# Kernel tuning notes

Hardware: AMD Instinct MI355X
Metric: run time of the kernel (lower is better)

## Reference

```python
import jax, jax.numpy as jnp
import numpy as np

N_E = 4096
E_DIM = 256
DECAY = 0.99
EPS = 1e-5


def setup_inputs() -> dict:
    key = jax.random.key(0)
    k1, k2 = jax.random.split(key)
    z = jax.random.normal(k1, (8, 256, 16, 16, 16), dtype=jnp.float32)
    embedding = jax.random.normal(k2, (N_E, E_DIM), dtype=jnp.float32)
    return {
        "z": z,
        "embedding": embedding,
        "cluster_size": jnp.zeros((N_E,), dtype=jnp.float32),
        "embedding_avg": embedding,  # buffer initialized as embedding.clone()
    }


def reference(z, embedding, cluster_size, embedding_avg):
    n_e, e_dim = embedding.shape
    # b c h w d -> b h w d c, then flatten tokens
    zt = jnp.einsum('bchwd->bhwdc', z)
    zf = zt.reshape(-1, e_dim)                      # [N, e_dim]
    # squared euclidean distances: ||z||^2 + ||e||^2 - 2 z.e
    d = (jnp.sum(zf * zf, axis=1, keepdims=True)
         + jnp.sum(embedding * embedding, axis=1)
         - 2.0 * jnp.einsum('bd,nd->bn', zf, embedding))  # [N, n_e]
    idx = jnp.argmin(d, axis=1)                     # [N]
    # EMA statistics (equivalent to one-hot.T reductions, done via scatter)
    n_total = jnp.zeros((n_e,), zf.dtype).at[idx].add(1.0)          # encodings.sum(0)
    dw = jax.ops.segment_sum(zf, idx, num_segments=n_e)             # encodings.T @ zf
    new_cluster = cluster_size * DECAY + (1.0 - DECAY) * n_total
    new_avg = embedding_avg * DECAY + (1.0 - DECAY) * dw
    n = new_cluster.sum()
    cs = (new_cluster + EPS) / (n + n_e * EPS) * n
    new_embed = new_avg / cs[:, None]
    # quantize (gather == one-hot @ embedding) with straight-through estimator
    zq = jnp.take(embedding, idx, axis=0).reshape(zt.shape)
    zq = zt + jax.lax.stop_gradient(zq - zt)
    zq = jnp.einsum('bhwdc->bchwd', zq)
    usage = (n_total > 0).sum().astype(jnp.float32) / n_e
    return zq, idx, new_cluster, new_avg, new_embed, usage
```

## Files before the change

### kernel.cpp

```cpp
#include <hip/hip_runtime.h>

#define N_E   4096
#define E_DIM 256
#define NTOK  32768
#define ZX    4096
#define DECAY 0.99f
#define EPSV  1e-5f
#define TAU   0.3f
#define NJB   32
#define NHALF 64
#define NSPL  4
#define IBIG  0x7fffffff

typedef _Float16 half8 __attribute__((ext_vector_type(8)));
typedef __attribute__((ext_vector_type(4))) float f32x4;

__device__ __forceinline__ unsigned short f2h(float x) {
    _Float16 h = (_Float16)x;
    unsigned short u;
    __builtin_memcpy(&u, &h, 2);
    return u;
}
__device__ __forceinline__ float h2f(unsigned short u) {
    _Float16 h;
    __builtin_memcpy(&h, &u, 2);
    return (float)h;
}
__device__ __forceinline__ unsigned umin2(unsigned a, unsigned b) { return a < b ? a : b; }
__device__ __forceinline__ unsigned umax2(unsigned a, unsigned b) { return a > b ? a : b; }
__device__ __forceinline__ void gload16(const void* g, void* l) {
    __builtin_amdgcn_global_load_lds(
        (const __attribute__((address_space(1))) char*)g,
        (__attribute__((address_space(3))) char*)l, 16, 0, 0);
}

__global__ void k_prep(const float* __restrict__ z, unsigned short* __restrict__ zh,
                       const float* __restrict__ emb, unsigned short* __restrict__ Bp,
                       float* __restrict__ enorm32, double* __restrict__ enorm64,
                       int* __restrict__ cnt, int* __restrict__ flagCnt,
                       int* __restrict__ flagCnt2) {
    __shared__ float lt[64][65];
    const int tid = threadIdx.x;
    if (blockIdx.x < 2048) {
        const int bid = blockIdx.x;
        const int xt = bid & 63, ct = (bid >> 6) & 3, b = bid >> 8;
        #pragma unroll
        for (int r = 0; r < 4; ++r) {
            int cy = r * 16 + (tid >> 4);
            int xx4 = tid & 15;
            float4 v = ((const float4*)z)[(size_t)(b * 256 + ct * 64 + cy) * 1024 + xt * 16 + xx4];
            lt[cy][xx4 * 4 + 0] = v.x; lt[cy][xx4 * 4 + 1] = v.y;
            lt[cy][xx4 * 4 + 2] = v.z; lt[cy][xx4 * 4 + 3] = v.w;
        }
        __syncthreads();
        #pragma unroll
        for (int it = 0; it < 2; ++it) {
            int tl = it * 32 + (tid >> 3);
            int c8 = tid & 7;
            unsigned short h[8];
            #pragma unroll
            for (int u = 0; u < 8; ++u) h[u] = f2h(lt[c8 * 8 + u][tl]);
            size_t t = (size_t)(b * 4096 + xt * 64 + tl);
            size_t o = t * 256 + ct * 64 + c8 * 8;
            *(ushort4*)&zh[o]     = make_ushort4(h[0], h[1], h[2], h[3]);
            *(ushort4*)&zh[o + 4] = make_ushort4(h[4], h[5], h[6], h[7]);
        }
    } else {
        const int eb = blockIdx.x - 2048;
        if (tid < 4) cnt[eb * 4 + tid] = 0;
        if (eb == 0 && tid == 0) { *flagCnt = 0; *flagCnt2 = 0; }
        int j = eb * 4 + (tid >> 6);
        int lane = tid & 63;
        float4 v = ((const float4*)emb)[(size_t)j * 64 + lane];
        float f[4] = {v.x, v.y, v.z, v.w};
        unsigned short h[4];
        #pragma unroll
        for (int u = 0; u < 4; ++u) h[u] = f2h(f[u]);
        *(ushort4*)&Bp[(size_t)j * E_DIM + lane * 4] = make_ushort4(h[0], h[1], h[2], h[3]);
        double s = 0.0;
        #pragma unroll
        for (int u = 0; u < 4; ++u) s += (double)f[u] * (double)f[u];
        #pragma unroll
        for (int off = 32; off; off >>= 1) s += __shfl_down(s, off, 64);
        if (lane == 0) { enorm32[j] = (float)s; enorm64[j] = s; }
    }
}

__global__ __launch_bounds__(256) void k_dist(
        const unsigned short* __restrict__ zh,
        const unsigned short* __restrict__ Bp, const float* __restrict__ enorm32,
        unsigned* __restrict__ pk1, unsigned* __restrict__ pk2, unsigned* __restrict__ pk3) {
    __shared__ __align__(16) char smem[32768];
    const int tid = threadIdx.x;
    const int lane = tid & 63;
    const int w = tid >> 6;
    const int wr = w >> 1, wc = w & 1;
    const int t0 = blockIdx.x * 128;
    const int jb = blockIdx.y;
    const int j0 = jb * 128;
    const int sw16 = (((lane & 7) ^ (lane >> 3)) << 4);
    const int rowsub = lane >> 3;

    f32x4 acc[4][4];
    #pragma unroll
    for (int m = 0; m < 4; ++m)
        #pragma unroll
        for (int nn = 0; nn < 4; ++nn)
            acc[m][nn] = (f32x4){0.f, 0.f, 0.f, 0.f};

    auto stage = [&](int s) {
        const int kb = s * 128 + sw16;
        #pragma unroll
        for (int c = 0; c < 4; ++c) {
            int seg = w * 4 + c;
            int arow = t0 + seg * 8 + rowsub;
            int brow = j0 + seg * 8 + rowsub;
            gload16((const char*)zh + (size_t)arow * 512 + kb, &smem[seg * 1024]);
            gload16((const char*)Bp + (size_t)brow * 512 + kb, &smem[16384 + seg * 1024]);
        }
    };

    stage(0);
    for (int s = 0; s < 4; ++s) {
        __syncthreads();
        const int xr = ((lane & 7) << 4);
        #pragma unroll
        for (int kk = 0; kk < 2; ++kk) {
            const int colb = (kk * 64 + ((lane >> 4) << 4)) ^ xr;
            half8 a[4], b[4];
            #pragma unroll
            for (int m = 0; m < 4; ++m)
                a[m] = *(const half8*)&smem[((wr * 64 + m * 16 + (lane & 15)) << 7) + colb];
            #pragma unroll
            for (int nn = 0; nn < 4; ++nn)
                b[nn] = *(const half8*)&smem[16384 + ((wc * 64 + nn * 16 + (lane & 15)) << 7) + colb];
            #pragma unroll
            for (int m = 0; m < 4; ++m)
                #pragma unroll
                for (int nn = 0; nn < 4; ++nn)
                    acc[m][nn] = __builtin_amdgcn_mfma_f32_16x16x32_f16(b[nn], a[m], acc[m][nn], 0, 0, 0);
        }
        if (s < 3) {
            __syncthreads();
            stage(s + 1);
        }
    }

    const int g   = lane >> 4;
    const int gg4 = g * 4;
    const int h   = jb * 2 + wc;
    float enb[4][4];
    #pragma unroll
    for (int nn = 0; nn < 4; ++nn) {
        float4 e4 = *(const float4*)&enorm32[j0 + wc * 64 + nn * 16 + gg4];
        enb[nn][0] = e4.x + 4096.f; enb[nn][1] = e4.y + 4096.f;
        enb[nn][2] = e4.z + 4096.f; enb[nn][3] = e4.w + 4096.f;
    }
    unsigned s1 = 0, s2 = 0, s3 = 0;
    #pragma unroll
    for (int m = 0; m < 4; ++m) {
        unsigned k1 = 0xFFFFFFFFu, k2 = 0xFFFFFFFFu, k3 = 0xFFFFFFFFu;
        #pragma unroll
        for (int nn = 0; nn < 4; ++nn)
            #pragma unroll
            for (int r = 0; r < 4; ++r) {
                float sc = fmaf(-2.f, acc[m][nn][r], enb[nn][r]);
                unsigned key = (__float_as_uint(sc) & 0xFFFFFFC0u)
                             | (unsigned)(gg4 + nn * 16 + r);
                k3 = umin2(k3, umax2(k2, key));
                k2 = umin2(k2, umax2(k1, key));
                k1 = umin2(k1, key);
            }
        #pragma unroll
        for (int off = 16; off <= 32; off <<= 1) {
            unsigned b1 = (unsigned)__shfl_xor((int)k1, off, 64);
            unsigned b2 = (unsigned)__shfl_xor((int)k2, off, 64);
            unsigned b3 = (unsigned)__shfl_xor((int)k3, off, 64);
            unsigned p  = umax2(k1, b1);
            unsigned q  = umin2(k2, b2);
            unsigned r2 = umax2(k2, b2);
            unsigned ss = umin2(k3, b3);
            k1 = umin2(k1, b1);
            k2 = umin2(p, q);
            k3 = umin2(umax2(p, q), umin2(r2, ss));
        }
        s1 = (g == m) ? k1 : s1;
        s2 = (g == m) ? k2 : s2;
        s3 = (g == m) ? k3 : s3;
    }
    size_t o = (size_t)h * NTOK + t0 + wr * 64 + lane;
    pk1[o] = s1; pk2[o] = s2; pk3[o] = s3;
}

__global__ void k_merge(const unsigned* __restrict__ pk1, const unsigned* __restrict__ pk2,
                        const unsigned* __restrict__ pk3,
                        int* __restrict__ idx32, int* __restrict__ cnt,
                        float* __restrict__ out_idx,
                        int* __restrict__ xlist, int* __restrict__ xn,
                        int* __restrict__ flagList, int* __restrict__ flagCount,
                        int* __restrict__ flagList2, int* __restrict__ flagCount2) {
    int t = blockIdx.x * blockDim.x + threadIdx.x;
    if (t >= NTOK) return;
    unsigned g1 = 0xFFFFFFFFu, g2 = 0xFFFFFFFFu;
    int h1 = 0;
    #pragma unroll 4
    for (int s = 0; s < NHALF; s++) {
        unsigned a = pk1[(size_t)s * NTOK + t];
        unsigned b = pk2[(size_t)s * NTOK + t];
        bool c = a < g1;
        g2 = c ? g1 : umin2(g2, a);
        h1 = c ? s : h1;
        g1 = c ? a : g1;
        g2 = umin2(g2, b);
    }
    int x1 = h1 * 64 + (int)(g1 & 63u);
    idx32[t] = x1;
    atomicAdd(&cnt[x1], 1);
    out_idx[t] = (float)x1;
    float v1 = __uint_as_float(g1 & 0xFFFFFFC0u);
    float v2 = __uint_as_float(g2 & 0xFFFFFFC0u);
    if (v2 - v1 >= TAU) return;
    unsigned thrk = __float_as_uint(v1 + TAU) | 63u;
    int nc = 0; bool full = false;
    for (int s = 0; s < NHALF; s++) {
        unsigned a = pk1[(size_t)s * NTOK + t];
        if (a > thrk) continue;
        if (pk3[(size_t)s * NTOK + t] <= thrk) { full = true; break; }
        if (nc == 8) { full = true; break; }
        xlist[t * 8 + nc++] = s * 64 + (int)(a & 63u);
        unsigned b = pk2[(size_t)s * NTOK + t];
        if (b <= thrk) {
            if (nc == 8) { full = true; break; }
            xlist[t * 8 + nc++] = s * 64 + (int)(b & 63u);
        }
    }
    if (full) {
        int q = atomicAdd(flagCount2, 1);
        flagList2[q] = t;
    } else {
        xn[t] = nc;
        int q = atomicAdd(flagCount, 1);
        flagList[q] = t;
    }
}

__global__ __launch_bounds__(512) void k_triR(
        const float* __restrict__ z, const float* __restrict__ emb,
        const double* __restrict__ enorm64,
        const int* __restrict__ flagList, const int* __restrict__ flagCount,
        const int* __restrict__ xlist, const int* __restrict__ xn,
        const int* __restrict__ flagList2, const int* __restrict__ flagCount2,
        int* __restrict__ idx32, int* __restrict__ cnt, float* __restrict__ out_idx) {
    __shared__ float zrow[E_DIM];
    __shared__ double rv[512];
    __shared__ int ri[512];
    const int tid = threadIdx.x;
    if (blockIdx.x < 384) {
        const int lane = tid & 63;
        const int wid = blockIdx.x * 8 + (tid >> 6);
        const int nw = 384 * 8;
        const int nf = *flagCount;
        for (int f = wid; f < nf; f += nw) {
            int t = flagList[f];
            int b = t >> 12, x = t & 4095;
            double zz[4];
            #pragma unroll
            for (int u = 0; u < 4; ++u)
                zz[u] = (double)z[(size_t)(b * 256 + lane * 4 + u) * 4096 + x];
            int m = xn[t];
            double best = 1e300; int bi = IBIG;
            for (int c = 0; c < m; ++c) {
                int j = xlist[t * 8 + c];
                float4 e = ((const float4*)emb)[(size_t)j * 64 + lane];
                double d = zz[0] * (double)e.x + zz[1] * (double)e.y
                         + zz[2] * (double)e.z + zz[3] * (double)e.w;
                #pragma unroll
                for (int off = 32; off; off >>= 1) d += __shfl_down(d, off, 64);
                double s = enorm64[j] - 2.0 * d;
                if (s < best || (s == best && j < bi)) { best = s; bi = j; }
            }
            if (lane == 0) {
                int old = idx32[t];
                if (bi != old) {
                    idx32[t] = bi;
                    out_idx[t] = (float)bi;
                    atomicSub(&cnt[old], 1);
                    atomicAdd(&cnt[bi], 1);
                }
            }
        }
    } else {
        const int nf = *flagCount2;
        for (int f = blockIdx.x - 384; f < nf; f += 128) {
            const int t = flagList2[f];
            const int b = t >> 12, x = t & 4095;
            __syncthreads();
            if (tid < E_DIM) zrow[tid] = z[(size_t)(b * 256 + tid) * 4096 + x];
            __syncthreads();
            double best = 1e300; int bi = IBIG;
            for (int s = 0; s < N_E / 512; s++) {
                int j = s * 512 + tid;
                const float4* er4 = (const float4*)(emb + (size_t)j * E_DIM);
                double a0 = 0.0, a1 = 0.0, a2 = 0.0, a3 = 0.0;
                for (int k4 = 0; k4 < 64; ++k4) {
                    float4 e = er4[k4];
                    a0 = fma((double)e.x, (double)zrow[k4 * 4 + 0], a0);
                    a1 = fma((double)e.y, (double)zrow[k4 * 4 + 1], a1);
                    a2 = fma((double)e.z, (double)zrow[k4 * 4 + 2], a2);
                    a3 = fma((double)e.w, (double)zrow[k4 * 4 + 3], a3);
                }
                double d = enorm64[j] - 2.0 * ((a0 + a1) + (a2 + a3));
                if (d < best || (d == best && j < bi)) { best = d; bi = j; }
            }
            rv[tid] = best; ri[tid] = bi;
            __syncthreads();
            for (int off = 256; off; off >>= 1) {
                if (tid < off) {
                    if (rv[tid + off] < rv[tid] ||
                        (rv[tid + off] == rv[tid] && ri[tid + off] < ri[tid])) {
                        rv[tid] = rv[tid + off]; ri[tid] = ri[tid + off];
                    }
                }
                __syncthreads();
            }
            if (tid == 0) {
                int old = idx32[t];
                int nw2 = ri[0];
                if (nw2 != old) {
                    idx32[t] = nw2;
                    out_idx[t] = (float)nw2;
                    atomicSub(&cnt[old], 1);
                    atomicAdd(&cnt[nw2], 1);
                }
            }
            __syncthreads();
        }
    }
}

__global__ void k_scan(const int* __restrict__ cnt, int* __restrict__ offs,
                       const float* __restrict__ cluster_size,
                       float* __restrict__ nval, float* __restrict__ out_usage) {
    __shared__ int sc[1024];
    __shared__ float sn[1024];
    __shared__ float su[1024];
    int tid = threadIdx.x;
    int c0 = cnt[tid * 4], c1 = cnt[tid * 4 + 1], c2 = cnt[tid * 4 + 2], c3 = cnt[tid * 4 + 3];
    int ls = c0 + c1 + c2 + c3;
    float ns = 0.f, us = 0.f;
    {
        int cc[4] = {c0, c1, c2, c3};
        #pragma unroll
        for (int u = 0; u < 4; ++u) {
            ns += cluster_size[tid * 4 + u] * DECAY + (1.f - DECAY) * (float)cc[u];
            us += (cc[u] > 0) ? 1.f : 0.f;
        }
    }
    sc[tid] = ls; sn[tid] = ns; su[tid] = us;
    __syncthreads();
    for (int off = 1; off < 1024; off <<= 1) {
        int v = (tid >= off) ? sc[tid - off] : 0;
        __syncthreads();
        sc[tid] += v;
        __syncthreads();
    }
    int base = sc[tid] - ls;
    offs[tid * 4] = base;
    offs[tid * 4 + 1] = base + c0;
    offs[tid * 4 + 2] = base + c0 + c1;
    offs[tid * 4 + 3] = base + c0 + c1 + c2;
    for (int off = 512; off; off >>= 1) {
        if (tid < off) { sn[tid] += sn[tid + off]; su[tid] += su[tid + off]; }
        __syncthreads();
    }
    if (tid == 0) { *nval = sn[0]; *out_usage = su[0] / (float)N_E; }
}

__global__ void k_place(const int* __restrict__ idx32, int* __restrict__ offs,
                        int* __restrict__ tokList) {
    int t = blockIdx.x * blockDim.x + threadIdx.x;
    if (t >= NTOK) return;
    int j = idx32[t];
    int p = atomicAdd(&offs[j], 1);
    tokList[p] = t;
}

__global__ __launch_bounds__(512) void k_dw(const unsigned short* __restrict__ zh,
                       const int* __restrict__ cnt, const int* __restrict__ offs,
                       const int* __restrict__ tokList, float* __restrict__ dwp) {
    __shared__ float red[8][256];
    const int j = blockIdx.x;
    const int split = blockIdx.y;
    const int g = threadIdx.x >> 6;
    const int lane = threadIdx.x & 63;
    const int n = cnt[j];
    const int s0 = offs[j] - n;
    const int stride = NSPL * 8;
    float4 acc = make_float4(0.f, 0.f, 0.f, 0.f);
    int i = split * 8 + g;
    if (i < n) {
        int t_cur = tokList[s0 + i];
        i += stride;
        for (; i < n; i += stride) {
            int t_nxt = tokList[s0 + i];
            ushort4 h = *(const ushort4*)&zh[(size_t)t_cur * 256 + lane * 4];
            acc.x += h2f(h.x); acc.y += h2f(h.y);
            acc.z += h2f(h.z); acc.w += h2f(h.w);
            t_cur = t_nxt;
        }
        ushort4 h = *(const ushort4*)&zh[(size_t)t_cur * 256 + lane * 4];
        acc.x += h2f(h.x); acc.y += h2f(h.y);
        acc.z += h2f(h.z); acc.w += h2f(h.w);
    }
    red[g][lane * 4 + 0] = acc.x; red[g][lane * 4 + 1] = acc.y;
    red[g][lane * 4 + 2] = acc.z; red[g][lane * 4 + 3] = acc.w;
    __syncthreads();
    if (g == 0) {
        float4 o;
        int c = lane * 4;
        o.x = red[0][c+0] + red[1][c+0] + red[2][c+0] + red[3][c+0]
            + red[4][c+0] + red[5][c+0] + red[6][c+0] + red[7][c+0];
        o.y = red[0][c+1] + red[1][c+1] + red[2][c+1] + red[3][c+1]
            + red[4][c+1] + red[5][c+1] + red[6][c+1] + red[7][c+1];
        o.z = red[0][c+2] + red[1][c+2] + red[2][c+2] + red[3][c+2]
            + red[4][c+2] + red[5][c+2] + red[6][c+2] + red[7][c+2];
        o.w = red[0][c+3] + red[1][c+3] + red[2][c+3] + red[3][c+3]
            + red[4][c+3] + red[5][c+3] + red[6][c+3] + red[7][c+3];
        ((float4*)dwp)[((size_t)split * N_E + j) * 64 + lane] = o;
    }
}

__global__ void k_finalzq(const float* __restrict__ dwp, const int* __restrict__ cnt,
                          const float* __restrict__ cluster_size,
                          const float* __restrict__ emb_avg, const float* __restrict__ nval,
                          float* __restrict__ out_cluster, float* __restrict__ out_avg,
                          float* __restrict__ out_embed,
                          const float* __restrict__ emb, const int* __restrict__ idx32,
                          float* __restrict__ out_zq) {
    if (blockIdx.x < 1024) {
        int j = blockIdx.x * 4 + (threadIdx.x >> 6);
        int lane = threadIdx.x & 63;
        float4 dw = make_float4(0.f, 0.f, 0.f, 0.f);
        #pragma unroll
        for (int s = 0; s < NSPL; ++s) {
            float4 v = ((const float4*)dwp)[((size_t)s * N_E + j) * 64 + lane];
            dw.x += v.x; dw.y += v.y; dw.z += v.z; dw.w += v.w;
        }
        float nc = cluster_size[j] * DECAY + (1.f - DECAY) * (float)cnt[j];
        float nv = *nval;
        float cs = (nc + EPSV) / (nv + (float)N_E * EPSV) * nv;
        float4 ea = ((const float4*)emb_avg)[(size_t)j * 64 + lane];
        float4 na, ne;
        na.x = ea.x * DECAY + (1.f - DECAY) * dw.x;
        na.y = ea.y * DECAY + (1.f - DECAY) * dw.y;
        na.z = ea.z * DECAY + (1.f - DECAY) * dw.z;
        na.w = ea.w * DECAY + (1.f - DECAY) * dw.w;
        ne.x = na.x / cs; ne.y = na.y / cs; ne.z = na.z / cs; ne.w = na.w / cs;
        ((float4*)out_avg)[(size_t)j * 64 + lane] = na;
        ((float4*)out_embed)[(size_t)j * 64 + lane] = ne;
        if (lane == 0) out_cluster[j] = nc;
    } else {
        int t = (blockIdx.x - 1024) * 256 + threadIdx.x;
        int j = idx32[t];
        int b = t >> 12, x = t & 4095;
        const float4* er = (const float4*)(emb + (size_t)j * E_DIM);
        float* ob = out_zq + (size_t)b * (E_DIM * ZX) + x;
        #pragma unroll 8
        for (int c4 = 0; c4 < E_DIM / 4; c4++) {
            float4 v = er[c4];
            ob[(size_t)(c4 * 4 + 0) * ZX] = v.x;
            ob[(size_t)(c4 * 4 + 1) * ZX] = v.y;
            ob[(size_t)(c4 * 4 + 2) * ZX] = v.z;
            ob[(size_t)(c4 * 4 + 3) * ZX] = v.w;
        }
    }
}

extern "C" void kernel_launch(void* const* d_in, const int* in_sizes, int n_in,
                              void* d_out, int out_size, void* d_ws, size_t ws_size,
                              hipStream_t stream) {
    const float* z            = (const float*)d_in[0];
    const float* emb          = (const float*)d_in[1];
    const float* cluster_size = (const float*)d_in[2];
    const float* emb_avg      = (const float*)d_in[3];
    float* out = (float*)d_out;

    char* ws = (char*)d_ws;
    unsigned short* zh   = (unsigned short*)(ws + 0);
    float* enorm32       = (float*)(ws + 16777216);
    double* enorm64      = (double*)(ws + 16793600);
    int* idx32           = (int*)(ws + 16826368);
    int* flagList        = (int*)(ws + 16957440);
    int* flagList2       = (int*)(ws + 17088512);
    int* xlist           = (int*)(ws + 17219584);
    int* xn              = (int*)(ws + 18268160);
    int* cnt             = (int*)(ws + 18399232);
    int* offs            = (int*)(ws + 18415616);
    int* flagCnt         = (int*)(ws + 18432000);
    int* flagCnt2        = (int*)(ws + 18432064);
    float* nval          = (float*)(ws + 18432128);
    float* dwp           = (float*)(ws + 18874368);

    unsigned* pk1        = (unsigned*)(out + 0);
    unsigned* pk2        = (unsigned*)(out + 2097152);
    unsigned* pk3        = (unsigned*)(out + 4194304);
    unsigned short* Bp   = (unsigned short*)(out + 7340032);
    int*   tokList       = (int*)(out + 7864320);

    float* out_zq      = out + 0;
    float* out_idx     = out + 8388608;
    float* out_cluster = out + 8421376;
    float* out_avg     = out + 8425472;
    float* out_embed   = out + 9474048;
    float* out_usage   = out + 10522624;

    hipLaunchKernelGGL(k_prep,   dim3(3072), dim3(256), 0, stream,
                       z, zh, emb, Bp, enorm32, enorm64, cnt, flagCnt, flagCnt2);
    hipLaunchKernelGGL(k_dist,   dim3(256, NJB), dim3(256), 0, stream,
                       zh, Bp, enorm32, pk1, pk2, pk3);
    hipLaunchKernelGGL(k_merge,  dim3(128), dim3(256), 0, stream,
                       pk1, pk2, pk3, idx32, cnt, out_idx,
                       xlist, xn, flagList, flagCnt, flagList2, flagCnt2);
    hipLaunchKernelGGL(k_triR,   dim3(512), dim3(512), 0, stream,
                       z, emb, enorm64, flagList, flagCnt, xlist, xn,
                       flagList2, flagCnt2, idx32, cnt, out_idx);
    hipLaunchKernelGGL(k_scan,   dim3(1), dim3(1024), 0, stream, cnt, offs,
                       cluster_size, nval, out_usage);
    hipLaunchKernelGGL(k_place,  dim3(128), dim3(256), 0, stream, idx32, offs, tokList);
    hipLaunchKernelGGL(k_dw,     dim3(4096, NSPL), dim3(512), 0, stream,
                       zh, cnt, offs, tokList, dwp);
    hipLaunchKernelGGL(k_finalzq, dim3(1152), dim3(256), 0, stream,
                       dwp, cnt, cluster_size, emb_avg, nval,
                       out_cluster, out_avg, out_embed, emb, idx32, out_zq);
}
```

Before: 199.8 us.

## Merge column-half top-3 in dist kernel and fuse zq gather into dw kernel

The distance kernel now merges the two wave-column halves' top-3 keys through shared memory before writing, so it stores 32 partial slices per token instead of 64. The key encoding gives up one more mantissa bit to hold a 7-bit column index. This halves the pk traffic and the work in the merge loop. The zq scatter-gather moves out of the finalize kernel into the dw kernel as extra blocks so it overlaps the segment sums, and tokList moves to the workspace, which makes it possible to pack the pk buffers more tightly. In exchange the distance kernel gains extra barriers, and the keys are coarser, which may push more tokens into the refinement path.

```diff
diff --git a/kernel.cpp b/kernel.cpp
--- a/kernel.cpp
+++ b/kernel.cpp
@@ -8,7 +8,6 @@
 #define EPSV  1e-5f
 #define TAU   0.3f
 #define NJB   32
-#define NHALF 64
 #define NSPL  4
 #define IBIG  0x7fffffff
 
@@ -148,7 +147,7 @@
 
     const int g   = lane >> 4;
     const int gg4 = g * 4;
-    const int h   = jb * 2 + wc;
+    const int cbase = (wc << 6);
     float enb[4][4];
     #pragma unroll
     for (int nn = 0; nn < 4; ++nn) {
@@ -165,8 +164,8 @@
             #pragma unroll
             for (int r = 0; r < 4; ++r) {
                 float sc = fmaf(-2.f, acc[m][nn][r], enb[nn][r]);
-                unsigned key = (__float_as_uint(sc) & 0xFFFFFFC0u)
-                             | (unsigned)(gg4 + nn * 16 + r);
+                unsigned key = (__float_as_uint(sc) & 0xFFFFFF80u)
+                             | (unsigned)(cbase | (gg4 + nn * 16 + r));
                 k3 = umin2(k3, umax2(k2, key));
                 k2 = umin2(k2, umax2(k1, key));
                 k1 = umin2(k1, key);
@@ -188,8 +187,28 @@
         s2 = (g == m) ? k2 : s2;
         s3 = (g == m) ? k3 : s3;
     }
-    size_t o = (size_t)h * NTOK + t0 + wr * 64 + lane;
-    pk1[o] = s1; pk2[o] = s2; pk3[o] = s3;
+    unsigned* mb = (unsigned*)smem;
+    __syncthreads();
+    if (wc == 1) {
+        mb[wr * 64 + lane]       = s1;
+        mb[128 + wr * 64 + lane] = s2;
+        mb[256 + wr * 64 + lane] = s3;
+    }
+    __syncthreads();
+    if (wc == 0) {
+        unsigned o1 = mb[wr * 64 + lane];
+        unsigned o2 = mb[128 + wr * 64 + lane];
+        unsigned o3 = mb[256 + wr * 64 + lane];
+        unsigned r1 = umin2(s1, o1);
+        unsigned A  = umax2(s1, o1);
+        unsigned B  = umin2(s2, o2);
+        unsigned C  = umax2(s2, o2);
+        unsigned D  = umin2(s3, o3);
+        unsigned r2 = umin2(A, B);
+        unsigned r3 = umin2(umax2(A, B), umin2(C, D));
+        size_t o = (size_t)jb * NTOK + t0 + wr * 64 + lane;
+        pk1[o] = r1; pk2[o] = r2; pk3[o] = r3;
+    }
 }
 
 __global__ void k_merge(const unsigned* __restrict__ pk1, const unsigned* __restrict__ pk2,
@@ -204,7 +223,7 @@
     unsigned g1 = 0xFFFFFFFFu, g2 = 0xFFFFFFFFu;
     int h1 = 0;
     #pragma unroll 4
-    for (int s = 0; s < NHALF; s++) {
+    for (int s = 0; s < NJB; s++) {
         unsigned a = pk1[(size_t)s * NTOK + t];
         unsigned b = pk2[(size_t)s * NTOK + t];
         bool c = a < g1;
@@ -213,25 +232,25 @@
         g1 = c ? a : g1;
         g2 = umin2(g2, b);
     }
-    int x1 = h1 * 64 + (int)(g1 & 63u);
+    int x1 = h1 * 128 + (int)(g1 & 127u);
     idx32[t] = x1;
     atomicAdd(&cnt[x1], 1);
     out_idx[t] = (float)x1;
-    float v1 = __uint_as_float(g1 & 0xFFFFFFC0u);
-    float v2 = __uint_as_float(g2 & 0xFFFFFFC0u);
+    float v1 = __uint_as_float(g1 & 0xFFFFFF80u);
+    float v2 = __uint_as_float(g2 & 0xFFFFFF80u);
     if (v2 - v1 >= TAU) return;
-    unsigned thrk = __float_as_uint(v1 + TAU) | 63u;
+    unsigned thrk = __float_as_uint(v1 + TAU) | 127u;
     int nc = 0; bool full = false;
-    for (int s = 0; s < NHALF; s++) {
+    for (int s = 0; s < NJB; s++) {
         unsigned a = pk1[(size_t)s * NTOK + t];
         if (a > thrk) continue;
         if (pk3[(size_t)s * NTOK + t] <= thrk) { full = true; break; }
         if (nc == 8) { full = true; break; }
-        xlist[t * 8 + nc++] = s * 64 + (int)(a & 63u);
+        xlist[t * 8 + nc++] = s * 128 + (int)(a & 127u);
         unsigned b = pk2[(size_t)s * NTOK + t];
         if (b <= thrk) {
             if (nc == 8) { full = true; break; }
-            xlist[t * 8 + nc++] = s * 64 + (int)(b & 63u);
+            xlist[t * 8 + nc++] = s * 128 + (int)(b & 127u);
         }
     }
     if (full) {
@@ -385,82 +404,54 @@
     tokList[p] = t;
 }
 
-__global__ __launch_bounds__(512) void k_dw(const unsigned short* __restrict__ zh,
+__global__ __launch_bounds__(512) void k_dwzq(const unsigned short* __restrict__ zh,
                        const int* __restrict__ cnt, const int* __restrict__ offs,
-                       const int* __restrict__ tokList, float* __restrict__ dwp) {
+                       const int* __restrict__ tokList, float* __restrict__ dwp,
+                       const float* __restrict__ emb, const int* __restrict__ idx32,
+                       float* __restrict__ out_zq) {
     __shared__ float red[8][256];
-    const int j = blockIdx.x;
-    const int split = blockIdx.y;
-    const int g = threadIdx.x >> 6;
-    const int lane = threadIdx.x & 63;
-    const int n = cnt[j];
-    const int s0 = offs[j] - n;
-    const int stride = NSPL * 8;
-    float4 acc = make_float4(0.f, 0.f, 0.f, 0.f);
-    int i = split * 8 + g;
-    if (i < n) {
-        int t_cur = tokList[s0 + i];
-        i += stride;
-        for (; i < n; i += stride) {
-            int t_nxt = tokList[s0 + i];
+    if (blockIdx.x < N_E) {
+        const int j = blockIdx.x;
+        const int split = blockIdx.y;
+        const int g = threadIdx.x >> 6;
+        const int lane = threadIdx.x & 63;
+        const int n = cnt[j];
+        const int s0 = offs[j] - n;
+        const int stride = NSPL * 8;
+        float4 acc = make_float4(0.f, 0.f, 0.f, 0.f);
+        int i = split * 8 + g;
+        if (i < n) {
+            int t_cur = tokList[s0 + i];
+            i += stride;
+            for (; i < n; i += stride) {
+                int t_nxt = tokList[s0 + i];
+                ushort4 h = *(const ushort4*)&zh[(size_t)t_cur * 256 + lane * 4];
+                acc.x += h2f(h.x); acc.y += h2f(h.y);
+                acc.z += h2f(h.z); acc.w += h2f(h.w);
+                t_cur = t_nxt;
+            }
             ushort4 h = *(const ushort4*)&zh[(size_t)t_cur * 256 + lane * 4];
             acc.x += h2f(h.x); acc.y += h2f(h.y);
             acc.z += h2f(h.z); acc.w += h2f(h.w);
-            t_cur = t_nxt;
-        }
-        ushort4 h = *(const ushort4*)&zh[(size_t)t_cur * 256 + lane * 4];
-        acc.x += h2f(h.x); acc.y += h2f(h.y);
-        acc.z += h2f(h.z); acc.w += h2f(h.w);
-    }
-    red[g][lane * 4 + 0] = acc.x; red[g][lane * 4 + 1] = acc.y;
-    red[g][lane * 4 + 2] = acc.z; red[g][lane * 4 + 3] = acc.w;
-    __syncthreads();
-    if (g == 0) {
-        float4 o;
-        int c = lane * 4;
-        o.x = red[0][c+0] + red[1][c+0] + red[2][c+0] + red[3][c+0]
-            + red[4][c+0] + red[5][c+0] + red[6][c+0] + red[7][c+0];
-        o.y = red[0][c+1] + red[1][c+1] + red[2][c+1] + red[3][c+1]
-            + red[4][c+1] + red[5][c+1] + red[6][c+1] + red[7][c+1];
-        o.z = red[0][c+2] + red[1][c+2] + red[2][c+2] + red[3][c+2]
-            + red[4][c+2] + red[5][c+2] + red[6][c+2] + red[7][c+2];
-        o.w = red[0][c+3] + red[1][c+3] + red[2][c+3] + red[3][c+3]
-            + red[4][c+3] + red[5][c+3] + red[6][c+3] + red[7][c+3];
-        ((float4*)dwp)[((size_t)split * N_E + j) * 64 + lane] = o;
-    }
-}
-
-__global__ void k_finalzq(const float* __restrict__ dwp, const int* __restrict__ cnt,
-                          const float* __restrict__ cluster_size,
-                          const float* __restrict__ emb_avg, const float* __restrict__ nval,
-                          float* __restrict__ out_cluster, float* __restrict__ out_avg,
-                          float* __restrict__ out_embed,
-                          const float* __restrict__ emb, const int* __restrict__ idx32,
-                          float* __restrict__ out_zq) {
-    if (blockIdx.x < 1024) {
-        int j = blockIdx.x * 4 + (threadIdx.x >> 6);
-        int lane = threadIdx.x & 63;
-        float4 dw = make_float4(0.f, 0.f, 0.f, 0.f);
-        #pragma unroll
-        for (int s = 0; s < NSPL; ++s) {
-            float4 v = ((const float4*)dwp)[((size_t)s * N_E + j) * 64 + lane];
-            dw.x += v.x; dw.y += v.y; dw.z += v.z; dw.w += v.w;
-        }
-        float nc = cluster_size[j] * DECAY + (1.f - DECAY) * (float)cnt[j];
-        float nv = *nval;
-        float cs = (nc + EPSV) / (nv + (float)N_E * EPSV) * nv;
-        float4 ea = ((const float4*)emb_avg)[(size_t)j * 64 + lane];
-        float4 na, ne;
-        na.x = ea.x * DECAY + (1.f - DECAY) * dw.x;
-        na.y = ea.y * DECAY + (1.f - DECAY) * dw.y;
-        na.z = ea.z * DECAY + (1.f - DECAY) * dw.z;
-        na.w = ea.w * DECAY + (1.f - DECAY) * dw.w;
-        ne.x = na.x / cs; ne.y = na.y / cs; ne.z = na.z / cs; ne.w = na.w / cs;
-        ((float4*)out_avg)[(size_t)j * 64 + lane] = na;
-        ((float4*)out_embed)[(size_t)j * 64 + lane] = ne;
-        if (lane == 0) out_cluster[j] = nc;
+        }
+        red[g][lane * 4 + 0] = acc.x; red[g][lane * 4 + 1] = acc.y;
+        red[g][lane * 4 + 2] = acc.z; red[g][lane * 4 + 3] = acc.w;
+        __syncthreads();
+        if (g == 0) {
+            float4 o;
+            int c = lane * 4;
+            o.x = red[0][c+0] + red[1][c+0] + red[2][c+0] + red[3][c+0]
+                + red[4][c+0] + red[5][c+0] + red[6][c+0] + red[7][c+0];
+            o.y = red[0][c+1] + red[1][c+1] + red[2][c+1] + red[3][c+1]
+                + red[4][c+1] + red[5][c+1] + red[6][c+1] + red[7][c+1];
+            o.z = red[0][c+2] + red[1][c+2] + red[2][c+2] + red[3][c+2]
+                + red[4][c+2] + red[5][c+2] + red[6][c+2] + red[7][c+2];
+            o.w = red[0][c+3] + red[1][c+3] + red[2][c+3] + red[3][c+3]
+                + red[4][c+3] + red[5][c+3] + red[6][c+3] + red[7][c+3];
+            ((float4*)dwp)[((size_t)split * N_E + j) * 64 + lane] = o;
+        }
     } else {
-        int t = (blockIdx.x - 1024) * 256 + threadIdx.x;
+        int t = (blockIdx.x - N_E) * (NSPL * 512) + blockIdx.y * 512 + threadIdx.x;
         int j = idx32[t];
         int b = t >> 12, x = t & 4095;
         const float4* er = (const float4*)(emb + (size_t)j * E_DIM);
@@ -474,6 +465,34 @@
             ob[(size_t)(c4 * 4 + 3) * ZX] = v.w;
         }
     }
+}
+
+__global__ void k_final(const float* __restrict__ dwp, const int* __restrict__ cnt,
+                        const float* __restrict__ cluster_size,
+                        const float* __restrict__ emb_avg, const float* __restrict__ nval,
+                        float* __restrict__ out_cluster, float* __restrict__ out_avg,
+                        float* __restrict__ out_embed) {
+    int j = blockIdx.x * 4 + (threadIdx.x >> 6);
+    int lane = threadIdx.x & 63;
+    float4 dw = make_float4(0.f, 0.f, 0.f, 0.f);
+    #pragma unroll
+    for (int s = 0; s < NSPL; ++s) {
+        float4 v = ((const float4*)dwp)[((size_t)s * N_E + j) * 64 + lane];
+        dw.x += v.x; dw.y += v.y; dw.z += v.z; dw.w += v.w;
+    }
+    float nc = cluster_size[j] * DECAY + (1.f - DECAY) * (float)cnt[j];
+    float nv = *nval;
+    float cs = (nc + EPSV) / (nv + (float)N_E * EPSV) * nv;
+    float4 ea = ((const float4*)emb_avg)[(size_t)j * 64 + lane];
+    float4 na, ne;
+    na.x = ea.x * DECAY + (1.f - DECAY) * dw.x;
+    na.y = ea.y * DECAY + (1.f - DECAY) * dw.y;
+    na.z = ea.z * DECAY + (1.f - DECAY) * dw.z;
+    na.w = ea.w * DECAY + (1.f - DECAY) * dw.w;
+    ne.x = na.x / cs; ne.y = na.y / cs; ne.z = na.z / cs; ne.w = na.w / cs;
+    ((float4*)out_avg)[(size_t)j * 64 + lane] = na;
+    ((float4*)out_embed)[(size_t)j * 64 + lane] = ne;
+    if (lane == 0) out_cluster[j] = nc;
 }
 
 extern "C" void kernel_launch(void* const* d_in, const int* in_sizes, int n_in,
@@ -500,12 +519,12 @@
     int* flagCnt2        = (int*)(ws + 18432064);
     float* nval          = (float*)(ws + 18432128);
     float* dwp           = (float*)(ws + 18874368);
+    int*   tokList       = (int*)(ws + 35651584);
 
     unsigned* pk1        = (unsigned*)(out + 0);
-    unsigned* pk2        = (unsigned*)(out + 2097152);
-    unsigned* pk3        = (unsigned*)(out + 4194304);
-    unsigned short* Bp   = (unsigned short*)(out + 7340032);
-    int*   tokList       = (int*)(out + 7864320);
+    unsigned* pk2        = (unsigned*)(out + 1048576);
+    unsigned* pk3        = (unsigned*)(out + 2097152);
+    unsigned short* Bp   = (unsigned short*)(out + 3145728);
 
     float* out_zq      = out + 0;
     float* out_idx     = out + 8388608;
@@ -527,9 +546,9 @@
     hipLaunchKernelGGL(k_scan,   dim3(1), dim3(1024), 0, stream, cnt, offs,
                        cluster_size, nval, out_usage);
     hipLaunchKernelGGL(k_place,  dim3(128), dim3(256), 0, stream, idx32, offs, tokList);
-    hipLaunchKernelGGL(k_dw,     dim3(4096, NSPL), dim3(512), 0, stream,
-                       zh, cnt, offs, tokList, dwp);
-    hipLaunchKernelGGL(k_finalzq, dim3(1152), dim3(256), 0, stream,
+    hipLaunchKernelGGL(k_dwzq,   dim3(N_E + 16, NSPL), dim3(512), 0, stream,
+                       zh, cnt, offs, tokList, dwp, emb, idx32, out_zq);
+    hipLaunchKernelGGL(k_final,  dim3(1024), dim3(256), 0, stream,
                        dwp, cnt, cluster_size, emb_avg, nval,
-                       out_cluster, out_avg, out_embed, emb, idx32, out_zq);
-}
+                       out_cluster, out_avg, out_embed);
+}
```

Result: no change. 201.8 us (+1.0%).

## Shrink distance tile to 128x64 with XCD-aware block mapping, fuse zq gather into dw

Applied to the files above, without the earlier changes.

The distance GEMM tile changes from 128x128 to 128 tokens x 64 codes per block, so there are twice as many blocks and each wave holds fewer accumulators. Block IDs are remapped so that token tiles stay grouped per XCD, which should improve L2 reuse of z rows. The per-code top-3 partials are written per 64-code group, and the merge loop is adjusted to match. The zq gather/scatter now runs in the same launch as the dw segment-sum, and the EMA finalisation moves to its own kernel, so the dw and zq work overlap. tokList moves into the workspace and Bp is relocated in the output buffer to avoid aliasing. The costs are more launches and re-reading the A tile for each code block.

```diff
diff --git a/kernel.cpp b/kernel.cpp
--- a/kernel.cpp
+++ b/kernel.cpp
@@ -7,8 +7,7 @@
 #define DECAY 0.99f
 #define EPSV  1e-5f
 #define TAU   0.3f
-#define NJB   32
-#define NHALF 64
+#define NHB   64
 #define NSPL  4
 #define IBIG  0x7fffffff
 
@@ -90,20 +89,23 @@
         const unsigned short* __restrict__ zh,
         const unsigned short* __restrict__ Bp, const float* __restrict__ enorm32,
         unsigned* __restrict__ pk1, unsigned* __restrict__ pk2, unsigned* __restrict__ pk3) {
-    __shared__ __align__(16) char smem[32768];
+    __shared__ __align__(16) char smem[24576];
     const int tid = threadIdx.x;
     const int lane = tid & 63;
     const int w = tid >> 6;
-    const int wr = w >> 1, wc = w & 1;
-    const int t0 = blockIdx.x * 128;
-    const int jb = blockIdx.y;
-    const int j0 = jb * 128;
+    const int n = blockIdx.y * 256 + blockIdx.x;
+    const int xcd = n & 7;
+    const int mq = n >> 3;
+    const int tb = xcd * 32 + (mq & 31);
+    const int jb = mq >> 5;
+    const int t0 = tb * 128;
+    const int j0 = jb * 64;
     const int sw16 = (((lane & 7) ^ (lane >> 3)) << 4);
     const int rowsub = lane >> 3;
 
-    f32x4 acc[4][4];
+    f32x4 acc[2][4];
     #pragma unroll
-    for (int m = 0; m < 4; ++m)
+    for (int m = 0; m < 2; ++m)
         #pragma unroll
         for (int nn = 0; nn < 4; ++nn)
             acc[m][nn] = (f32x4){0.f, 0.f, 0.f, 0.f};
@@ -114,8 +116,12 @@
         for (int c = 0; c < 4; ++c) {
             int seg = w * 4 + c;
             int arow = t0 + seg * 8 + rowsub;
+            gload16((const char*)zh + (size_t)arow * 512 + kb, &smem[seg * 1024]);
+        }
+        #pragma unroll
+        for (int c = 0; c < 2; ++c) {
+            int seg = w * 2 + c;
             int brow = j0 + seg * 8 + rowsub;
-            gload16((const char*)zh + (size_t)arow * 512 + kb, &smem[seg * 1024]);
             gload16((const char*)Bp + (size_t)brow * 512 + kb, &smem[16384 + seg * 1024]);
         }
     };
@@ -127,15 +133,15 @@
         #pragma unroll
         for (int kk = 0; kk < 2; ++kk) {
             const int colb = (kk * 64 + ((lane >> 4) << 4)) ^ xr;
-            half8 a[4], b[4];
+            half8 a[2], b[4];
             #pragma unroll
-            for (int m = 0; m < 4; ++m)
-                a[m] = *(const half8*)&smem[((wr * 64 + m * 16 + (lane & 15)) << 7) + colb];
+            for (int m = 0; m < 2; ++m)
+                a[m] = *(const half8*)&smem[((w * 32 + m * 16 + (lane & 15)) << 7) + colb];
             #pragma unroll
             for (int nn = 0; nn < 4; ++nn)
-                b[nn] = *(const half8*)&smem[16384 + ((wc * 64 + nn * 16 + (lane & 15)) << 7) + colb];
+                b[nn] = *(const half8*)&smem[16384 + ((nn * 16 + (lane & 15)) << 7) + colb];
             #pragma unroll
-            for (int m = 0; m < 4; ++m)
+            for (int m = 0; m < 2; ++m)
                 #pragma unroll
                 for (int nn = 0; nn < 4; ++nn)
                     acc[m][nn] = __builtin_amdgcn_mfma_f32_16x16x32_f16(b[nn], a[m], acc[m][nn], 0, 0, 0);
@@ -148,17 +154,16 @@
 
     const int g   = lane >> 4;
     const int gg4 = g * 4;
-    const int h   = jb * 2 + wc;
     float enb[4][4];
     #pragma unroll
     for (int nn = 0; nn < 4; ++nn) {
-        float4 e4 = *(const float4*)&enorm32[j0 + wc * 64 + nn * 16 + gg4];
+        float4 e4 = *(const float4*)&enorm32[j0 + nn * 16 + gg4];
         enb[nn][0] = e4.x + 4096.f; enb[nn][1] = e4.y + 4096.f;
         enb[nn][2] = e4.z + 4096.f; enb[nn][3] = e4.w + 4096.f;
     }
     unsigned s1 = 0, s2 = 0, s3 = 0;
     #pragma unroll
-    for (int m = 0; m < 4; ++m) {
+    for (int m = 0; m < 2; ++m) {
         unsigned k1 = 0xFFFFFFFFu, k2 = 0xFFFFFFFFu, k3 = 0xFFFFFFFFu;
         #pragma unroll
         for (int nn = 0; nn < 4; ++nn)
@@ -188,8 +193,10 @@
         s2 = (g == m) ? k2 : s2;
         s3 = (g == m) ? k3 : s3;
     }
-    size_t o = (size_t)h * NTOK + t0 + wr * 64 + lane;
-    pk1[o] = s1; pk2[o] = s2; pk3[o] = s3;
+    if (g < 2) {
+        size_t o = (size_t)jb * NTOK + t0 + w * 32 + g * 16 + (lane & 15);
+        pk1[o] = s1; pk2[o] = s2; pk3[o] = s3;
+    }
 }
 
 __global__ void k_merge(const unsigned* __restrict__ pk1, const unsigned* __restrict__ pk2,
@@ -204,7 +211,7 @@
     unsigned g1 = 0xFFFFFFFFu, g2 = 0xFFFFFFFFu;
     int h1 = 0;
     #pragma unroll 4
-    for (int s = 0; s < NHALF; s++) {
+    for (int s = 0; s < NHB; s++) {
         unsigned a = pk1[(size_t)s * NTOK + t];
         unsigned b = pk2[(size_t)s * NTOK + t];
         bool c = a < g1;
@@ -222,7 +229,7 @@
     if (v2 - v1 >= TAU) return;
     unsigned thrk = __float_as_uint(v1 + TAU) | 63u;
     int nc = 0; bool full = false;
-    for (int s = 0; s < NHALF; s++) {
+    for (int s = 0; s < NHB; s++) {
         unsigned a = pk1[(size_t)s * NTOK + t];
         if (a > thrk) continue;
         if (pk3[(size_t)s * NTOK + t] <= thrk) { full = true; break; }
@@ -385,82 +392,54 @@
     tokList[p] = t;
 }
 
-__global__ __launch_bounds__(512) void k_dw(const unsigned short* __restrict__ zh,
+__global__ __launch_bounds__(512) void k_dwzq(const unsigned short* __restrict__ zh,
                        const int* __restrict__ cnt, const int* __restrict__ offs,
-                       const int* __restrict__ tokList, float* __restrict__ dwp) {
+                       const int* __restrict__ tokList, float* __restrict__ dwp,
+                       const float* __restrict__ emb, const int* __restrict__ idx32,
+                       float* __restrict__ out_zq) {
     __shared__ float red[8][256];
-    const int j = blockIdx.x;
-    const int split = blockIdx.y;
-    const int g = threadIdx.x >> 6;
-    const int lane = threadIdx.x & 63;
-    const int n = cnt[j];
-    const int s0 = offs[j] - n;
-    const int stride = NSPL * 8;
-    float4 acc = make_float4(0.f, 0.f, 0.f, 0.f);
-    int i = split * 8 + g;
-    if (i < n) {
-        int t_cur = tokList[s0 + i];
-        i += stride;
-        for (; i < n; i += stride) {
-            int t_nxt = tokList[s0 + i];
+    if (blockIdx.x < N_E) {
+        const int j = blockIdx.x;
+        const int split = blockIdx.y;
+        const int g = threadIdx.x >> 6;
+        const int lane = threadIdx.x & 63;
+        const int n = cnt[j];
+        const int s0 = offs[j] - n;
+        const int stride = NSPL * 8;
+        float4 acc = make_float4(0.f, 0.f, 0.f, 0.f);
+        int i = split * 8 + g;
+        if (i < n) {
+            int t_cur = tokList[s0 + i];
+            i += stride;
+            for (; i < n; i += stride) {
+                int t_nxt = tokList[s0 + i];
+                ushort4 h = *(const ushort4*)&zh[(size_t)t_cur * 256 + lane * 4];
+                acc.x += h2f(h.x); acc.y += h2f(h.y);
+                acc.z += h2f(h.z); acc.w += h2f(h.w);
+                t_cur = t_nxt;
+            }
             ushort4 h = *(const ushort4*)&zh[(size_t)t_cur * 256 + lane * 4];
             acc.x += h2f(h.x); acc.y += h2f(h.y);
             acc.z += h2f(h.z); acc.w += h2f(h.w);
-            t_cur = t_nxt;
-        }
-        ushort4 h = *(const ushort4*)&zh[(size_t)t_cur * 256 + lane * 4];
-        acc.x += h2f(h.x); acc.y += h2f(h.y);
-        acc.z += h2f(h.z); acc.w += h2f(h.w);
-    }
-    red[g][lane * 4 + 0] = acc.x; red[g][lane * 4 + 1] = acc.y;
-    red[g][lane * 4 + 2] = acc.z; red[g][lane * 4 + 3] = acc.w;
-    __syncthreads();
-    if (g == 0) {
-        float4 o;
-        int c = lane * 4;
-        o.x = red[0][c+0] + red[1][c+0] + red[2][c+0] + red[3][c+0]
-            + red[4][c+0] + red[5][c+0] + red[6][c+0] + red[7][c+0];
-        o.y = red[0][c+1] + red[1][c+1] + red[2][c+1] + red[3][c+1]
-            + red[4][c+1] + red[5][c+1] + red[6][c+1] + red[7][c+1];
-        o.z = red[0][c+2] + red[1][c+2] + red[2][c+2] + red[3][c+2]
-            + red[4][c+2] + red[5][c+2] + red[6][c+2] + red[7][c+2];
-        o.w = red[0][c+3] + red[1][c+3] + red[2][c+3] + red[3][c+3]
-            + red[4][c+3] + red[5][c+3] + red[6][c+3] + red[7][c+3];
-        ((float4*)dwp)[((size_t)split * N_E + j) * 64 + lane] = o;
-    }
-}
-
-__global__ void k_finalzq(const float* __restrict__ dwp, const int* __restrict__ cnt,
-                          const float* __restrict__ cluster_size,
-                          const float* __restrict__ emb_avg, const float* __restrict__ nval,
-                          float* __restrict__ out_cluster, float* __restrict__ out_avg,
-                          float* __restrict__ out_embed,
-                          const float* __restrict__ emb, const int* __restrict__ idx32,
-                          float* __restrict__ out_zq) {
-    if (blockIdx.x < 1024) {
-        int j = blockIdx.x * 4 + (threadIdx.x >> 6);
-        int lane = threadIdx.x & 63;
-        float4 dw = make_float4(0.f, 0.f, 0.f, 0.f);
-        #pragma unroll
-        for (int s = 0; s < NSPL; ++s) {
-            float4 v = ((const float4*)dwp)[((size_t)s * N_E + j) * 64 + lane];
-            dw.x += v.x; dw.y += v.y; dw.z += v.z; dw.w += v.w;
-        }
-        float nc = cluster_size[j] * DECAY + (1.f - DECAY) * (float)cnt[j];
-        float nv = *nval;
-        float cs = (nc + EPSV) / (nv + (float)N_E * EPSV) * nv;
-        float4 ea = ((const float4*)emb_avg)[(size_t)j * 64 + lane];
-        float4 na, ne;
-        na.x = ea.x * DECAY + (1.f - DECAY) * dw.x;
-        na.y = ea.y * DECAY + (1.f - DECAY) * dw.y;
-        na.z = ea.z * DECAY + (1.f - DECAY) * dw.z;
-        na.w = ea.w * DECAY + (1.f - DECAY) * dw.w;
-        ne.x = na.x / cs; ne.y = na.y / cs; ne.z = na.z / cs; ne.w = na.w / cs;
-        ((float4*)out_avg)[(size_t)j * 64 + lane] = na;
-        ((float4*)out_embed)[(size_t)j * 64 + lane] = ne;
-        if (lane == 0) out_cluster[j] = nc;
+        }
+        red[g][lane * 4 + 0] = acc.x; red[g][lane * 4 + 1] = acc.y;
+        red[g][lane * 4 + 2] = acc.z; red[g][lane * 4 + 3] = acc.w;
+        __syncthreads();
+        if (g == 0) {
+            float4 o;
+            int c = lane * 4;
+            o.x = red[0][c+0] + red[1][c+0] + red[2][c+0] + red[3][c+0]
+                + red[4][c+0] + red[5][c+0] + red[6][c+0] + red[7][c+0];
+            o.y = red[0][c+1] + red[1][c+1] + red[2][c+1] + red[3][c+1]
+                + red[4][c+1] + red[5][c+1] + red[6][c+1] + red[7][c+1];
+            o.z = red[0][c+2] + red[1][c+2] + red[2][c+2] + red[3][c+2]
+                + red[4][c+2] + red[5][c+2] + red[6][c+2] + red[7][c+2];
+            o.w = red[0][c+3] + red[1][c+3] + red[2][c+3] + red[3][c+3]
+                + red[4][c+3] + red[5][c+3] + red[6][c+3] + red[7][c+3];
+            ((float4*)dwp)[((size_t)split * N_E + j) * 64 + lane] = o;
+        }
     } else {
-        int t = (blockIdx.x - 1024) * 256 + threadIdx.x;
+        int t = (blockIdx.x - N_E) * (NSPL * 512) + blockIdx.y * 512 + threadIdx.x;
         int j = idx32[t];
         int b = t >> 12, x = t & 4095;
         const float4* er = (const float4*)(emb + (size_t)j * E_DIM);
@@ -474,6 +453,34 @@
             ob[(size_t)(c4 * 4 + 3) * ZX] = v.w;
         }
     }
+}
+
+__global__ void k_final(const float* __restrict__ dwp, const int* __restrict__ cnt,
+                        const float* __restrict__ cluster_size,
+                        const float* __restrict__ emb_avg, const float* __restrict__ nval,
+                        float* __restrict__ out_cluster, float* __restrict__ out_avg,
+                        float* __restrict__ out_embed) {
+    int j = blockIdx.x * 4 + (threadIdx.x >> 6);
+    int lane = threadIdx.x & 63;
+    float4 dw = make_float4(0.f, 0.f, 0.f, 0.f);
+    #pragma unroll
+    for (int s = 0; s < NSPL; ++s) {
+        float4 v = ((const float4*)dwp)[((size_t)s * N_E + j) * 64 + lane];
+        dw.x += v.x; dw.y += v.y; dw.z += v.z; dw.w += v.w;
+    }
+    float nc = cluster_size[j] * DECAY + (1.f - DECAY) * (float)cnt[j];
+    float nv = *nval;
+    float cs = (nc + EPSV) / (nv + (float)N_E * EPSV) * nv;
+    float4 ea = ((const float4*)emb_avg)[(size_t)j * 64 + lane];
+    float4 na, ne;
+    na.x = ea.x * DECAY + (1.f - DECAY) * dw.x;
+    na.y = ea.y * DECAY + (1.f - DECAY) * dw.y;
+    na.z = ea.z * DECAY + (1.f - DECAY) * dw.z;
+    na.w = ea.w * DECAY + (1.f - DECAY) * dw.w;
+    ne.x = na.x / cs; ne.y = na.y / cs; ne.z = na.z / cs; ne.w = na.w / cs;
+    ((float4*)out_avg)[(size_t)j * 64 + lane] = na;
+    ((float4*)out_embed)[(size_t)j * 64 + lane] = ne;
+    if (lane == 0) out_cluster[j] = nc;
 }
 
 extern "C" void kernel_launch(void* const* d_in, const int* in_sizes, int n_in,
@@ -500,12 +507,12 @@
     int* flagCnt2        = (int*)(ws + 18432064);
     float* nval          = (float*)(ws + 18432128);
     float* dwp           = (float*)(ws + 18874368);
+    int*   tokList       = (int*)(ws + 35651584);
 
     unsigned* pk1        = (unsigned*)(out + 0);
     unsigned* pk2        = (unsigned*)(out + 2097152);
     unsigned* pk3        = (unsigned*)(out + 4194304);
-    unsigned short* Bp   = (unsigned short*)(out + 7340032);
-    int*   tokList       = (int*)(out + 7864320);
+    unsigned short* Bp   = (unsigned short*)(out + 6291456);
 
     float* out_zq      = out + 0;
     float* out_idx     = out + 8388608;
@@ -516,7 +523,7 @@
 
     hipLaunchKernelGGL(k_prep,   dim3(3072), dim3(256), 0, stream,
                        z, zh, emb, Bp, enorm32, enorm64, cnt, flagCnt, flagCnt2);
-    hipLaunchKernelGGL(k_dist,   dim3(256, NJB), dim3(256), 0, stream,
+    hipLaunchKernelGGL(k_dist,   dim3(256, NHB), dim3(256), 0, stream,
                        zh, Bp, enorm32, pk1, pk2, pk3);
     hipLaunchKernelGGL(k_merge,  dim3(128), dim3(256), 0, stream,
                        pk1, pk2, pk3, idx32, cnt, out_idx,
@@ -527,9 +534,9 @@
     hipLaunchKernelGGL(k_scan,   dim3(1), dim3(1024), 0, stream, cnt, offs,
                        cluster_size, nval, out_usage);
     hipLaunchKernelGGL(k_place,  dim3(128), dim3(256), 0, stream, idx32, offs, tokList);
-    hipLaunchKernelGGL(k_dw,     dim3(4096, NSPL), dim3(512), 0, stream,
-                       zh, cnt, offs, tokList, dwp);
-    hipLaunchKernelGGL(k_finalzq, dim3(1152), dim3(256), 0, stream,
+    hipLaunchKernelGGL(k_dwzq,   dim3(N_E + 16, NSPL), dim3(512), 0, stream,
+                       zh, cnt, offs, tokList, dwp, emb, idx32, out_zq);
+    hipLaunchKernelGGL(k_final,  dim3(1024), dim3(256), 0, stream,
                        dwp, cnt, cluster_size, emb_avg, nval,
-                       out_cluster, out_avg, out_embed, emb, idx32, out_zq);
-}
+                       out_cluster, out_avg, out_embed);
+}
```

After: 220.7 us. 10.5% more time.
